# Kernel tuning notes

Measured on AMD Instinct MI355X. Metric: run time of the kernel, lower is better.

Reference implementation:

```python
import jax, jax.numpy as jnp
import numpy as np

NS = 4; DM = 1024; NH = 16; DK = 64; DFF = 4096; ML = 2048
VS = 32000; VT = 32000; B = 2; LS = 512; LT = 512
SCALE = float(np.sqrt(DK))


def _pos_enc():
    # Faithful to the original (quirky) PositionalEncoder:
    # denum uses index i (not i//2); even dims get cos(0)+sin(pe)=1+sin(pe), odd get cos(pe).
    pos = jnp.arange(ML, dtype=jnp.float32)[:, None]              # [ML,1]
    i = jnp.arange(DM, dtype=jnp.float32)[None, :]                # [1,DM]
    denum = 10000.0 ** (2.0 * i / DM)
    pe = pos / denum                                              # [ML,DM]
    c = (jnp.arange(DM) % 2).astype(jnp.float32)[None, :]
    s = 1.0 - c
    return jnp.cos(c * pe) + jnp.sin(s * pe)


def _ln(x, g, b):
    m = x.mean(-1, keepdims=True)
    v = ((x - m) ** 2).mean(-1, keepdims=True)
    return g * (x - m) / jnp.sqrt(v + 1e-5) + b


def _mha(xq, xkv, qkv_w, qkv_b, o_w, o_b, causal):
    # torch.chunk along last dim == reshape [B,L,NH,DK] with contiguous head blocks
    q = (xq @ qkv_w[0] + qkv_b[0]).reshape(xq.shape[0], xq.shape[1], NH, DK)
    k = (xkv @ qkv_w[1] + qkv_b[1]).reshape(xkv.shape[0], xkv.shape[1], NH, DK)
    v = (xkv @ qkv_w[2] + qkv_b[2]).reshape(xkv.shape[0], xkv.shape[1], NH, DK)
    scores = jnp.einsum('bqhd,bkhd->bhqk', q, k) / SCALE
    if causal:
        lq, lk = q.shape[1], k.shape[1]
        m = jnp.arange(lk)[None, :] > jnp.arange(lq)[:, None]     # triu(diagonal=1)
        scores = jnp.where(m[None, None], -jnp.inf, scores)
    a = jax.nn.softmax(scores, axis=-1)
    o = jnp.einsum('bhqk,bkhd->bqhd', a, v).reshape(xq.shape[0], xq.shape[1], NH * DK)
    return o @ o_w + o_b


def setup_inputs() -> dict:
    key = jax.random.key(0)
    ks = iter(jax.random.split(key, 40))

    def n(shape):
        return jax.random.normal(next(ks), shape, dtype=jnp.float32) * 0.02

    inp = {
        's': jax.random.randint(next(ks), (B, LS), 0, VS),
        't': jax.random.randint(next(ks), (B, LT), 0, VT),
        'emb_s_w': n((VS, DM)),
        'emb_t_w': n((VT, DM)),
        'enc_qkv_w': n((NS, 3, DM, DM)), 'enc_qkv_b': n((NS, 3, DM)),
        'enc_o_w': n((NS, DM, DM)), 'enc_o_b': n((NS, DM)),
        'enc_ln_w': jnp.ones((NS, DM), jnp.float32), 'enc_ln_b': jnp.zeros((NS, DM), jnp.float32),
        'enc_w1': n((NS, DM, DFF)), 'enc_b1': n((NS, DFF)),
        'enc_w2': n((NS, DFF, DM)), 'enc_b2': n((NS, DM)),
        'dec_qkv1_w': n((NS, 3, DM, DM)), 'dec_qkv1_b': n((NS, 3, DM)),
        'dec_o1_w': n((NS, DM, DM)), 'dec_o1_b': n((NS, DM)),
        'dec_qkv2_w': n((NS, 3, DM, DM)), 'dec_qkv2_b': n((NS, 3, DM)),
        'dec_o2_w': n((NS, DM, DM)), 'dec_o2_b': n((NS, DM)),
        'dec_ln_w': jnp.ones((NS, DM), jnp.float32), 'dec_ln_b': jnp.zeros((NS, DM), jnp.float32),
        'dec_w1': n((NS, DM, DFF)), 'dec_b1': n((NS, DFF)),
        'dec_w2': n((NS, DFF, DM)), 'dec_b2': n((NS, DM)),
        'out_w': n((DM, VT)), 'out_b': n((VT,)),
    }
    return inp


def reference(s, t, emb_s_w, emb_t_w,
              enc_qkv_w, enc_qkv_b, enc_o_w, enc_o_b, enc_ln_w, enc_ln_b,
              enc_w1, enc_b1, enc_w2, enc_b2,
              dec_qkv1_w, dec_qkv1_b, dec_o1_w, dec_o1_b,
              dec_qkv2_w, dec_qkv2_b, dec_o2_w, dec_o2_b,
              dec_ln_w, dec_ln_b, dec_w1, dec_b1, dec_w2, dec_b2,
              out_w, out_b):
    pe = _pos_enc()
    e = emb_s_w[s] + pe[:s.shape[1]][None]   # dropout p=0 -> identity
    d = emb_t_w[t] + pe[:t.shape[1]][None]

    for i in range(NS):  # encoder stack
        a = _mha(e, e, enc_qkv_w[i], enc_qkv_b[i], enc_o_w[i], enc_o_b[i], False)
        e = _ln(a + e, enc_ln_w[i], enc_ln_b[i])
        f = jnp.maximum(e @ enc_w1[i] + enc_b1[i], 0.0) @ enc_w2[i] + enc_b2[i]
        e = _ln(f + e, enc_ln_w[i], enc_ln_b[i])

    for i in range(NS):  # decoder stack
        a1 = _mha(d, d, dec_qkv1_w[i], dec_qkv1_b[i], dec_o1_w[i], dec_o1_b[i], True)
        d1 = _ln(a1 + d, dec_ln_w[i], dec_ln_b[i])
        # original passes mask=-1, which is truthy -> causal mask in cross-attn too
        a2 = _mha(d1, e, dec_qkv2_w[i], dec_qkv2_b[i], dec_o2_w[i], dec_o2_b[i], True)
        d2 = _ln(a2 + d1, dec_ln_w[i], dec_ln_b[i])
        f = jnp.maximum(d2 @ dec_w1[i] + dec_b1[i], 0.0) @ dec_w2[i] + dec_b2[i]
        d = f + d2  # no final LayerNorm in decoder block (faithful)

    return d @ out_w + out_b
```

## Files before the change

kernel.cpp:

```cpp
#include <hip/hip_runtime.h>
#include <hip/hip_bf16.h>
#include <math.h>

#define NSL 4
#define DM 1024
#define NH 16
#define DKH 64
#define DFF 4096
#define BB 2
#define LL 512
#define VTOK 32000

typedef short s16x8 __attribute__((ext_vector_type(8)));
typedef float f32x4 __attribute__((ext_vector_type(4)));

__device__ __forceinline__ void gload16(const void* g, void* l) {
  __builtin_amdgcn_global_load_lds((__attribute__((address_space(1))) void*)g,
                                   (__attribute__((address_space(3))) void*)l, 16, 0, 0);
}

__global__ __launch_bounds__(256) void embed2_kernel(
    const int* __restrict__ toks, const int* __restrict__ tokt,
    const float* __restrict__ ws, const float* __restrict__ wt,
    float* __restrict__ eo, __hip_bfloat16* __restrict__ eobf,
    float* __restrict__ dco, __hip_bfloat16* __restrict__ dcobf) {
  const int which = blockIdx.y;
  const int* tok = which ? tokt : toks;
  const float* w = which ? wt : ws;
  float* o = which ? dco : eo;
  __hip_bfloat16* obf = which ? dcobf : eobf;
  const int idx = blockIdx.x * 256 + threadIdx.x;
  const int dim = idx & (DM - 1);
  const int pos = (idx >> 10) & (LL - 1);
  const int b   = idx >> 19;
  const int token = tok[b * LL + pos];
  const float denum = powf(10000.0f, (2.0f * (float)dim) / (float)DM);
  const float pe = (float)pos / denum;
  const float val = (dim & 1) ? cosf(pe) : (1.0f + sinf(pe));
  const float r = w[(size_t)token * DM + dim] + val;
  o[idx] = r;
  obf[idx] = __float2bfloat16(r);
}

struct TJobs {
  const float* src[8];
  __hip_bfloat16* dst[8];
  int K[8];
  int N[8];
  int tiles[8];
  int njobs;
};

__global__ __launch_bounds__(256) void transpose_multi(TJobs jobs) {
  __shared__ float tb[64][65];
  int t = blockIdx.x;
  int ji = 0;
  while (t >= jobs.tiles[ji]) { t -= jobs.tiles[ji]; ++ji; }
  const int K = jobs.K[ji], N = jobs.N[ji];
  const int tpx = N >> 6;
  const int tpm = tpx * (K >> 6);
  const int mat = t / tpm;
  const int t2 = t - mat * tpm;
  const float* src = jobs.src[ji] + (long)mat * K * N;
  __hip_bfloat16* dst = jobs.dst[ji] + (long)mat * K * N;
  const int n0 = (t2 % tpx) * 64, k0 = (t2 / tpx) * 64;
  const int lc = (threadIdx.x & 15) * 4;
  const int lr = threadIdx.x >> 4;
  #pragma unroll
  for (int u = 0; u < 4; ++u) {
    const int r = lr + u * 16;
    const float4 v = *(const float4*)(src + (long)(k0 + r) * N + n0 + lc);
    tb[r][lc + 0] = v.x; tb[r][lc + 1] = v.y; tb[r][lc + 2] = v.z; tb[r][lc + 3] = v.w;
  }
  __syncthreads();
  #pragma unroll
  for (int u = 0; u < 4; ++u) {
    const int r = lr + u * 16;
    ushort4 o;
    __hip_bfloat16 h0 = __float2bfloat16(tb[lc + 0][r]);
    __hip_bfloat16 h1 = __float2bfloat16(tb[lc + 1][r]);
    __hip_bfloat16 h2 = __float2bfloat16(tb[lc + 2][r]);
    __hip_bfloat16 h3 = __float2bfloat16(tb[lc + 3][r]);
    o.x = *(unsigned short*)&h0; o.y = *(unsigned short*)&h1;
    o.z = *(unsigned short*)&h2; o.w = *(unsigned short*)&h3;
    *(ushort4*)(dst + (long)(n0 + r) * K + k0 + lc) = o;
  }
}

template<int BM, int BN, int BK, int RELU, int OBF, int SWZ, int VTM, int BMAP, int NTC>
__global__ __launch_bounds__(256, 2) void gemm_mfma(
    const __hip_bfloat16* __restrict__ A, const __hip_bfloat16* __restrict__ BT,
    const float* __restrict__ bias, void* __restrict__ Cout,
    int K, int lda, int ldb, int ldc,
    const float* __restrict__ res, __hip_bfloat16* __restrict__ obf2,
    __hip_bfloat16* __restrict__ vt, int vt_off, long vt_stride) {
  constexpr int WR = BM / 2, WC = BN / 2;
  constexpr int MF = WR / 16, NF = WC / 16;
  constexpr int CHK = BK / 8;
  constexpr int RPC = 64 / CHK;
  constexpr int ACALLS = BM / RPC / 4, BCALLS = BN / RPC / 4;
  constexpr int NLOADS = ACALLS + BCALLS;
  constexpr int KSUB = BK / 32;
  constexpr int ABUF = BM * BK, BBUF = BN * BK;
  constexpr int STAGE_BYTES = 2 * (ABUF + BBUF) * 2;
  constexpr int TT_BYTES = (VTM != 0) ? (BM * BN * 2) : 0;
  constexpr int CF_BYTES = NTC ? ((BM / 2) * BN * 4) : 0;
  constexpr int SMEM_A = STAGE_BYTES > TT_BYTES ? STAGE_BYTES : TT_BYTES;
  constexpr int SMEM_BYTES = SMEM_A > CF_BYTES ? SMEM_A : CF_BYTES;
  __shared__ __align__(16) char smem[SMEM_BYTES];
  __hip_bfloat16* As = (__hip_bfloat16*)smem;
  __hip_bfloat16* Bs = (__hip_bfloat16*)(smem + (size_t)2 * ABUF * 2);
  unsigned short* TT = (unsigned short*)smem;

  int bx = blockIdx.x, by = blockIdx.y;
  if (SWZ) {
    const int gx = gridDim.x;
    const int nwg = gx * gridDim.y;
    const int id = by * gx + bx;
    const int qq = nwg >> 3;
    const int swz = (id & 7) * qq + (id >> 3);
    bx = swz % gx; by = swz / gx;
  }
  const int bm = by * BM, bn = bx * BN;
  const int tid = threadIdx.x, lane = tid & 63, wid = tid >> 6;
  const int wr = (wid >> 1) * WR, wc = (wid & 1) * WC;
  const int frow = lane & 15, fkc = lane >> 4;

  auto swz_chk = [](int c, int r) {
    if (BK == 32)      return c ^ ((r >> 1) & 3);
    else if (BK == 64) return c ^ (r & 7);
    else               return c ^ (r & 15);
  };

  const int s_row = lane / CHK;
  const int s_chk = lane % CHK;

  auto stageAB = [&](int buf, int k0) {
    #pragma unroll
    for (int c = 0; c < ACALLS; ++c) {
      const int R0 = (wid * ACALLS + c) * RPC;
      const int row = R0 + s_row;
      gload16(A + (long)(bm + row) * lda + k0 + swz_chk(s_chk, row) * 8,
              As + buf * ABUF + R0 * BK);
    }
    #pragma unroll
    for (int c = 0; c < BCALLS; ++c) {
      const int R0 = (wid * BCALLS + c) * RPC;
      const int row = R0 + s_row;
      gload16(BT + (long)(bn + row) * ldb + k0 + swz_chk(s_chk, row) * 8,
              Bs + buf * BBUF + R0 * BK);
    }
  };

  f32x4 acc[MF][NF] = {};
  const int nt = K / BK;
  stageAB(0, 0);
  for (int t = 0; t < nt; ++t) {
    const int cur = t & 1;
    const bool more = (t + 1 < nt);
    if (more) {
      stageAB(cur ^ 1, (t + 1) * BK);
      asm volatile("s_waitcnt vmcnt(%0)" :: "n"(NLOADS) : "memory");
    } else {
      asm volatile("s_waitcnt vmcnt(0)" ::: "memory");
    }
    __builtin_amdgcn_s_barrier();
    asm volatile("" ::: "memory");
    #pragma unroll
    for (int s = 0; s < KSUB; ++s) {
      s16x8 af[MF], bfr[NF];
      #pragma unroll
      for (int mm = 0; mm < MF; ++mm) {
        const int r = wr + mm * 16 + frow;
        af[mm] = *(const s16x8*)&As[cur * ABUF + r * BK + swz_chk(s * 4 + fkc, r) * 8];
      }
      #pragma unroll
      for (int nn = 0; nn < NF; ++nn) {
        const int r = wc + nn * 16 + frow;
        bfr[nn] = *(const s16x8*)&Bs[cur * BBUF + r * BK + swz_chk(s * 4 + fkc, r) * 8];
      }
      #pragma unroll
      for (int mm = 0; mm < MF; ++mm)
        #pragma unroll
        for (int nn = 0; nn < NF; ++nn)
          acc[mm][nn] = __builtin_amdgcn_mfma_f32_16x16x32_bf16(af[mm], bfr[nn], acc[mm][nn], 0, 0, 0);
    }
    asm volatile("s_waitcnt lgkmcnt(0)" ::: "memory");
    __builtin_amdgcn_s_barrier();
  }

  if (NTC) {
    float* CF = (float*)smem;
    #pragma unroll
    for (int half = 0; half < 2; ++half) {
      __syncthreads();
      if ((wid >> 1) == half) {
        #pragma unroll
        for (int mm = 0; mm < MF; ++mm)
          #pragma unroll
          for (int nn = 0; nn < NF; ++nn) {
            const int col = wc + nn * 16 + frow;
            const float bs = bias[bn + col];
            #pragma unroll
            for (int j = 0; j < 4; ++j)
              CF[(mm * 16 + fkc * 4 + j) * BN + col] = acc[mm][nn][j] + bs;
          }
      }
      __syncthreads();
      constexpr int NPASS = (BM / 2) * BN / 4 / 256;
      #pragma unroll
      for (int ps = 0; ps < NPASS; ++ps) {
        const int idx = tid * 4 + ps * 1024;
        const int row = idx / BN, col = idx % BN;
        const f32x4 v = *(const f32x4*)&CF[row * BN + col];
        __builtin_nontemporal_store(
            v, (f32x4*)((float*)Cout + (long)(bm + half * (BM / 2) + row) * ldc + bn + col));
      }
    }
    return;
  }

  bool vt_blk = false;
  if (VTM == 1) vt_blk = (bn >= vt_off);
  if (VTM == 2) vt_blk = (((bn >> 10) & 1) == 1);

  #pragma unroll
  for (int mm = 0; mm < MF; ++mm)
    #pragma unroll
    for (int nn = 0; nn < NF; ++nn) {
      const int row0 = bm + wr + mm * 16 + fkc * 4;
      const int col  = bn + wc + nn * 16 + frow;
      float bs;
      if (BMAP) bs = bias[(col >> 11) * 3 * DM + DM + (col & 2047)];
      else      bs = bias[col];
      float vv[4];
      #pragma unroll
      for (int j = 0; j < 4; ++j) {
        float v = acc[mm][nn][j] + bs;
        if (RELU) v = fmaxf(v, 0.0f);
        const long ci = (long)(row0 + j) * ldc + col;
        if (res) v += res[ci];
        if (OBF) ((__hip_bfloat16*)Cout)[ci] = __float2bfloat16(v);
        else     ((float*)Cout)[ci] = v;
        if (obf2) obf2[ci] = __float2bfloat16(v);
        vv[j] = v;
      }
      if (VTM != 0 && vt_blk) {
        const int dl  = wc + nn * 16 + frow;
        const int jl0 = (wr + mm * 16 + fkc * 4) ^ ((dl & 7) << 3);
        ushort4 pk;
        __hip_bfloat16 h0 = __float2bfloat16(vv[0]);
        __hip_bfloat16 h1 = __float2bfloat16(vv[1]);
        __hip_bfloat16 h2 = __float2bfloat16(vv[2]);
        __hip_bfloat16 h3 = __float2bfloat16(vv[3]);
        pk.x = *(unsigned short*)&h0; pk.y = *(unsigned short*)&h1;
        pk.z = *(unsigned short*)&h2; pk.w = *(unsigned short*)&h3;
        *(ushort4*)&TT[dl * BM + jl0] = pk;
      }
    }

  if (VTM != 0 && vt_blk) {
    __syncthreads();
    constexpr int TPR = BM / 8;
    constexpr int RPP = 256 / TPR;
    constexpr int NP  = BN / RPP;
    const int jj = (tid % TPR) * 8;
    const int b = bm >> 9;
    const int jbase = bm & (LL - 1);
    const __hip_bfloat16* vtp;
    int dg0;
    if (VTM == 2) {
      vtp = vt + (long)(bn >> 11) * vt_stride;
      dg0 = bn & 1023;
    } else {
      vtp = vt;
      dg0 = bn - vt_off;
    }
    #pragma unroll
    for (int u = 0; u < NP; ++u) {
      const int dl = (tid / TPR) + u * RPP;
      const s16x8 val = *(const s16x8*)&TT[dl * BM + (jj ^ ((dl & 7) << 3))];
      *(s16x8*)((__hip_bfloat16*)vtp + ((long)(b * DM + dg0 + dl)) * LL + jbase + jj) = val;
    }
  }
}

template<int CAUSAL>
__global__ __launch_bounds__(256) void flash_attn(
    const __hip_bfloat16* __restrict__ Q, int ldq,
    const __hip_bfloat16* __restrict__ K, int ldk,
    const __hip_bfloat16* __restrict__ VT,
    __hip_bfloat16* __restrict__ O) {
  __shared__ __align__(16) __hip_bfloat16 Ks[2][64 * 64];
  __shared__ __align__(16) __hip_bfloat16 Vs[2][64 * 64];
  __shared__ __align__(16) __hip_bfloat16 Ps[4][16 * 64];
  const int qt = blockIdx.x;
  const int bh = blockIdx.y;
  const int b = bh >> 4, h = bh & (NH - 1);
  const int tid = threadIdx.x, lane = tid & 63, wid = tid >> 6;
  const int frow = lane & 15, fg = lane >> 4;

  const __hip_bfloat16* Qb = Q + ((long)b * LL) * ldq + h * DKH;
  const __hip_bfloat16* Kb = K + ((long)b * LL) * ldk + h * DKH;
  const __hip_bfloat16* Vb = VT + (long)b * DM * LL + (long)(h * DKH) * LL;
  __hip_bfloat16* Ob = O + ((long)b * LL) * DM + h * DKH;

  auto stageKV = [&](int buf, int jt) {
    #pragma unroll
    for (int u = 0; u < 2; ++u) {
      const int R0 = (wid * 2 + u) * 8;
      const int row = R0 + (lane >> 3);
      const int cg = (lane & 7) ^ (row & 7);
      gload16(Kb + (long)(jt * 64 + row) * ldk + cg * 8, &Ks[buf][R0 * 64]);
      gload16(Vb + (long)row * LL + jt * 64 + cg * 8, &Vs[buf][R0 * 64]);
    }
  };

  const int qrow = qt * 64 + wid * 16 + frow;
  s16x8 aq[2];
  #pragma unroll
  for (int s = 0; s < 2; ++s)
    aq[s] = *(const s16x8*)(Qb + (long)qrow * ldq + s * 32 + fg * 8);

  f32x4 o[4] = {};
  float m[4], l[4];
  #pragma unroll
  for (int j = 0; j < 4; ++j) { m[j] = -INFINITY; l[j] = 0.0f; }

  const int ntiles = CAUSAL ? (qt + 1) : (LL / 64);
  stageKV(0, 0);
  for (int jt = 0; jt < ntiles; ++jt) {
    const int cur = jt & 1;
    const bool more = (jt + 1 < ntiles);
    if (more) {
      stageKV(cur ^ 1, jt + 1);
      asm volatile("s_waitcnt vmcnt(4)" ::: "memory");
    } else {
      asm volatile("s_waitcnt vmcnt(0)" ::: "memory");
    }
    __builtin_amdgcn_s_barrier();
    asm volatile("" ::: "memory");

    f32x4 sa[4] = {};
    __builtin_amdgcn_s_setprio(1);
    #pragma unroll
    for (int s = 0; s < 2; ++s)
      #pragma unroll
      for (int nf = 0; nf < 4; ++nf) {
        const int jr = nf * 16 + frow;
        const s16x8 kf = *(const s16x8*)&Ks[cur][jr * 64 + (((s * 4 + fg) ^ (jr & 7)) * 8)];
        sa[nf] = __builtin_amdgcn_mfma_f32_16x16x32_bf16(aq[s], kf, sa[nf], 0, 0, 0);
      }
    __builtin_amdgcn_s_setprio(0);
    #pragma unroll
    for (int nf = 0; nf < 4; ++nf)
      #pragma unroll
      for (int j = 0; j < 4; ++j) {
        float v = sa[nf][j] * 0.125f;
        if (CAUSAL) {
          const int r = qt * 64 + wid * 16 + fg * 4 + j;
          const int c = jt * 64 + nf * 16 + frow;
          if (c > r) v = -1e30f;
        }
        sa[nf][j] = v;
      }

    float fs[4];
    #pragma unroll
    for (int j = 0; j < 4; ++j) {
      float v = fmaxf(fmaxf(sa[0][j], sa[1][j]), fmaxf(sa[2][j], sa[3][j]));
      v = fmaxf(v, __shfl_xor(v, 1));
      v = fmaxf(v, __shfl_xor(v, 2));
      v = fmaxf(v, __shfl_xor(v, 4));
      v = fmaxf(v, __shfl_xor(v, 8));
      const float mn = fmaxf(m[j], v);
      fs[j] = __expf(m[j] - mn);
      m[j] = mn;
    }
    float rs[4] = {0.0f, 0.0f, 0.0f, 0.0f};
    #pragma unroll
    for (int nf = 0; nf < 4; ++nf)
      #pragma unroll
      for (int j = 0; j < 4; ++j) {
        const float p = __expf(sa[nf][j] - m[j]);
        sa[nf][j] = p;
        rs[j] += p;
      }
    #pragma unroll
    for (int j = 0; j < 4; ++j) {
      float v = rs[j];
      v += __shfl_xor(v, 1);
      v += __shfl_xor(v, 2);
      v += __shfl_xor(v, 4);
      v += __shfl_xor(v, 8);
      l[j] = l[j] * fs[j] + v;
      o[0][j] *= fs[j]; o[1][j] *= fs[j]; o[2][j] *= fs[j]; o[3][j] *= fs[j];
    }

    __hip_bfloat16* Pw = &Ps[wid][0];
    #pragma unroll
    for (int nf = 0; nf < 4; ++nf)
      #pragma unroll
      for (int j = 0; j < 4; ++j) {
        const int qr = fg * 4 + j;
        const int col = nf * 16 + frow;
        Pw[qr * 64 + (((col >> 3) ^ (qr & 7)) * 8) + (col & 7)] = __float2bfloat16(sa[nf][j]);
      }
    asm volatile("s_waitcnt lgkmcnt(0)" ::: "memory");

    __builtin_amdgcn_s_setprio(1);
    #pragma unroll
    for (int s = 0; s < 2; ++s) {
      const s16x8 pa = *(const s16x8*)&Pw[frow * 64 + (((s * 4 + fg) ^ (frow & 7)) * 8)];
      #pragma unroll
      for (int nf = 0; nf < 4; ++nf) {
        const int dr = nf * 16 + frow;
        const s16x8 vf = *(const s16x8*)&Vs[cur][dr * 64 + (((s * 4 + fg) ^ (dr & 7)) * 8)];
        o[nf] = __builtin_amdgcn_mfma_f32_16x16x32_bf16(pa, vf, o[nf], 0, 0, 0);
      }
    }
    __builtin_amdgcn_s_setprio(0);
    asm volatile("s_waitcnt lgkmcnt(0)" ::: "memory");
    __builtin_amdgcn_s_barrier();
  }

  #pragma unroll
  for (int nf = 0; nf < 4; ++nf)
    #pragma unroll
    for (int j = 0; j < 4; ++j) {
      const int row = qt * 64 + wid * 16 + fg * 4 + j;
      const int col = nf * 16 + frow;
      Ob[(long)row * DM + col] = __float2bfloat16(o[nf][j] / l[j]);
    }
}

__global__ __launch_bounds__(256) void add_ln1(
    const float* __restrict__ x,
    const float* __restrict__ g, const float* __restrict__ bta,
    float* __restrict__ out, __hip_bfloat16* __restrict__ obf) {
  __shared__ float red[256];
  const int tid = threadIdx.x;
  const size_t base = (size_t)blockIdx.x * DM;
  float v[4];
  #pragma unroll
  for (int u = 0; u < 4; ++u) v[u] = x[base + tid + u * 256];
  red[tid] = v[0] + v[1] + v[2] + v[3];
  __syncthreads();
  for (int s = 128; s > 0; s >>= 1) {
    if (tid < s) red[tid] += red[tid + s];
    __syncthreads();
  }
  const float mean = red[0] * (1.0f / DM);
  __syncthreads();
  float sq = 0.0f;
  #pragma unroll
  for (int u = 0; u < 4; ++u) { const float d = v[u] - mean; sq += d * d; }
  red[tid] = sq;
  __syncthreads();
  for (int s = 128; s > 0; s >>= 1) {
    if (tid < s) red[tid] += red[tid + s];
    __syncthreads();
  }
  const float rstd = rsqrtf(red[0] * (1.0f / DM) + 1e-5f);
  #pragma unroll
  for (int u = 0; u < 4; ++u) {
    const int c = tid + u * 256;
    const float o = g[c] * (v[u] - mean) * rstd + bta[c];
    out[base + c] = o;
    obf[base + c] = __float2bfloat16(o);
  }
}

template<int BM, int BN, int BK, int RELU, int OBF, int SWZ, int VTM, int BMAP, int NTC = 0>
static inline void launch_gemm(hipStream_t st, const __hip_bfloat16* A, const __hip_bfloat16* BT,
                               const float* bias, void* C, int M, int N, int K,
                               int lda, int ldb, int ldc,
                               const float* res = nullptr, __hip_bfloat16* obf2 = nullptr,
                               __hip_bfloat16* vt = nullptr, int vt_off = 0, long vt_stride = 0) {
  dim3 g(N / BN, M / BM);
  gemm_mfma<BM, BN, BK, RELU, OBF, SWZ, VTM, BMAP, NTC><<<g, 256, 0, st>>>(
      A, BT, bias, C, K, lda, ldb, ldc, res, obf2, vt, vt_off, vt_stride);
}

static inline void add_tjob(TJobs& J, int& total, const float* src, __hip_bfloat16* dst,
                            int K, int N, int nmat) {
  const int i = J.njobs++;
  J.src[i] = src; J.dst[i] = dst; J.K[i] = K; J.N[i] = N;
  J.tiles[i] = nmat * (N / 64) * (K / 64);
  total += J.tiles[i];
}

extern "C" void kernel_launch(void* const* d_in, const int* in_sizes, int n_in,
                              void* d_out, int out_size, void* d_ws, size_t ws_size,
                              hipStream_t stream) {
  (void)in_sizes; (void)n_in; (void)out_size; (void)ws_size;
  const int*   s          = (const int*)d_in[0];
  const int*   t          = (const int*)d_in[1];
  const float* emb_s_w    = (const float*)d_in[2];
  const float* emb_t_w    = (const float*)d_in[3];
  const float* enc_qkv_w  = (const float*)d_in[4];
  const float* enc_qkv_b  = (const float*)d_in[5];
  const float* enc_o_w    = (const float*)d_in[6];
  const float* enc_o_b    = (const float*)d_in[7];
  const float* enc_ln_w   = (const float*)d_in[8];
  const float* enc_ln_b   = (const float*)d_in[9];
  const float* enc_w1     = (const float*)d_in[10];
  const float* enc_b1     = (const float*)d_in[11];
  const float* enc_w2     = (const float*)d_in[12];
  const float* enc_b2     = (const float*)d_in[13];
  const float* dec_qkv1_w = (const float*)d_in[14];
  const float* dec_qkv1_b = (const float*)d_in[15];
  const float* dec_o1_w   = (const float*)d_in[16];
  const float* dec_o1_b   = (const float*)d_in[17];
  const float* dec_qkv2_w = (const float*)d_in[18];
  const float* dec_qkv2_b = (const float*)d_in[19];
  const float* dec_o2_w   = (const float*)d_in[20];
  const float* dec_o2_b   = (const float*)d_in[21];
  const float* dec_ln_w   = (const float*)d_in[22];
  const float* dec_ln_b   = (const float*)d_in[23];
  const float* dec_w1     = (const float*)d_in[24];
  const float* dec_b1     = (const float*)d_in[25];
  const float* dec_w2     = (const float*)d_in[26];
  const float* dec_b2     = (const float*)d_in[27];
  const float* out_w      = (const float*)d_in[28];
  const float* out_b      = (const float*)d_in[29];
  float* out = (float*)d_out;

  char* p = (char*)d_ws;
  auto alloc = [&](size_t bytes) {
    char* r = p; p += (bytes + 255) & ~(size_t)255; return (void*)r;
  };
  const size_t T = (size_t)BB * LL * DM;
  const size_t DD = (size_t)DM * DM, DF = (size_t)DM * DFF;
  float* e    = (float*)alloc(T * 4);
  float* dcur = (float*)alloc(T * 4);
  float* tmp  = (float*)alloc(T * 4);
  float* d1b  = (float*)alloc(T * 4);
  float* d2b  = (float*)alloc(T * 4);
  __hip_bfloat16* e_bf    = (__hip_bfloat16*)alloc(T * 2);
  __hip_bfloat16* dcur_bf = (__hip_bfloat16*)alloc(T * 2);
  __hip_bfloat16* d1b_bf  = (__hip_bfloat16*)alloc(T * 2);
  __hip_bfloat16* d2b_bf  = (__hip_bfloat16*)alloc(T * 2);
  __hip_bfloat16* q_bf    = (__hip_bfloat16*)alloc(T * 2);
  __hip_bfloat16* qkv_bf  = (__hip_bfloat16*)alloc((size_t)BB * LL * 3 * DM * 2);
  __hip_bfloat16* ab_bf   = (__hip_bfloat16*)alloc(T * 2);
  __hip_bfloat16* hid_bf  = (__hip_bfloat16*)alloc((size_t)BB * LL * DFF * 2);
  __hip_bfloat16* VT      = (__hip_bfloat16*)alloc((size_t)BB * DM * LL * 2);
  __hip_bfloat16* WT      = (__hip_bfloat16*)alloc((size_t)VTOK * DM * 2);
  __hip_bfloat16* WTq   = (__hip_bfloat16*)alloc(4 * DD * 2);
  __hip_bfloat16* WTkv  = (__hip_bfloat16*)alloc(8 * DD * 2);
  __hip_bfloat16* kvall = (__hip_bfloat16*)alloc((size_t)BB * LL * 8192 * 2);
  const long VT4S = (long)BB * DM * LL;
  __hip_bfloat16* VT4   = (__hip_bfloat16*)alloc(4 * VT4S * 2);

  const int M = BB * LL;

  embed2_kernel<<<dim3((int)(T / 256), 2), 256, 0, stream>>>(
      s, t, emb_s_w, emb_t_w, e, e_bf, dcur, dcur_bf);

  for (int i = 0; i < NSL; ++i) {
    TJobs J{}; int tot = 0;
    add_tjob(J, tot, enc_qkv_w + (size_t)i * 3 * DD, WT,            DM, DM, 3);
    add_tjob(J, tot, enc_o_w   + (size_t)i * DD,     WT + 3 * DD,   DM, DM, 1);
    add_tjob(J, tot, enc_w1    + (size_t)i * DF,     WT + 4 * DD,   DM, DFF, 1);
    add_tjob(J, tot, enc_w2    + (size_t)i * DF,     WT + 4 * DD + DF, DFF, DM, 1);
    transpose_multi<<<tot, 256, 0, stream>>>(J);

    launch_gemm<64, 64, 128, 0, 1, 0, 1, 0>(stream, e_bf, WT,
                                            enc_qkv_b + (size_t)i * 3 * DM, qkv_bf,
                                            M, 3 * DM, DM, DM, DM, 3 * DM,
                                            nullptr, nullptr, VT, 2 * DM);
    flash_attn<0><<<dim3(LL / 64, BB * NH), 256, 0, stream>>>(
        qkv_bf, 3 * DM, qkv_bf + DM, 3 * DM, VT, ab_bf);
    launch_gemm<64, 32, 128, 0, 0, 0, 0, 0>(stream, ab_bf, WT + 3 * DD,
                                            enc_o_b + (size_t)i * DM, tmp,
                                            M, DM, DM, DM, DM, DM, e);
    add_ln1<<<M, 256, 0, stream>>>(tmp, enc_ln_w + (size_t)i * DM, enc_ln_b + (size_t)i * DM, e, e_bf);
    launch_gemm<128, 64, 64, 1, 1, 0, 0, 0>(stream, e_bf, WT + 4 * DD,
                                            enc_b1 + (size_t)i * DFF, hid_bf,
                                            M, DFF, DM, DM, DM, DFF);
    launch_gemm<64, 32, 128, 0, 0, 0, 0, 0>(stream, hid_bf, WT + 4 * DD + DF,
                                            enc_b2 + (size_t)i * DM, tmp,
                                            M, DM, DFF, DFF, DFF, DM, e);
    add_ln1<<<M, 256, 0, stream>>>(tmp, enc_ln_w + (size_t)i * DM, enc_ln_b + (size_t)i * DM, e, e_bf);
  }

  {
    TJobs J{}; int tot = 0;
    for (int i = 0; i < NSL; ++i) {
      add_tjob(J, tot, dec_qkv2_w + (size_t)i * 3 * DD,      WTq  + (size_t)i * DD,     DM, DM, 1);
      add_tjob(J, tot, dec_qkv2_w + (size_t)i * 3 * DD + DD, WTkv + (size_t)i * 2 * DD, DM, DM, 2);
    }
    transpose_multi<<<tot, 256, 0, stream>>>(J);
    launch_gemm<128, 128, 32, 0, 1, 0, 2, 1>(stream, e_bf, WTkv, dec_qkv2_b, kvall,
                                             M, 8192, DM, DM, DM, 8192,
                                             nullptr, nullptr, VT4, 0, VT4S);
  }

  for (int i = 0; i < NSL; ++i) {
    TJobs J{}; int tot = 0;
    add_tjob(J, tot, dec_qkv1_w + (size_t)i * 3 * DD, WT,              DM, DM, 3);
    add_tjob(J, tot, dec_o1_w   + (size_t)i * DD,     WT + 3 * DD,     DM, DM, 1);
    add_tjob(J, tot, dec_o2_w   + (size_t)i * DD,     WT + 4 * DD,     DM, DM, 1);
    add_tjob(J, tot, dec_w1     + (size_t)i * DF,     WT + 5 * DD,     DM, DFF, 1);
    add_tjob(J, tot, dec_w2     + (size_t)i * DF,     WT + 5 * DD + DF, DFF, DM, 1);
    transpose_multi<<<tot, 256, 0, stream>>>(J);

    launch_gemm<64, 64, 128, 0, 1, 0, 1, 0>(stream, dcur_bf, WT,
                                            dec_qkv1_b + (size_t)i * 3 * DM, qkv_bf,
                                            M, 3 * DM, DM, DM, DM, 3 * DM,
                                            nullptr, nullptr, VT, 2 * DM);
    flash_attn<1><<<dim3(LL / 64, BB * NH), 256, 0, stream>>>(
        qkv_bf, 3 * DM, qkv_bf + DM, 3 * DM, VT, ab_bf);
    launch_gemm<64, 32, 128, 0, 0, 0, 0, 0>(stream, ab_bf, WT + 3 * DD,
                                            dec_o1_b + (size_t)i * DM, tmp,
                                            M, DM, DM, DM, DM, DM, dcur);
    add_ln1<<<M, 256, 0, stream>>>(tmp, dec_ln_w + (size_t)i * DM, dec_ln_b + (size_t)i * DM, d1b, d1b_bf);

    launch_gemm<64, 32, 128, 0, 1, 0, 0, 0>(stream, d1b_bf, WTq + (size_t)i * DD,
                                            dec_qkv2_b + (size_t)i * 3 * DM, q_bf,
                                            M, DM, DM, DM, DM, DM);
    flash_attn<1><<<dim3(LL / 64, BB * NH), 256, 0, stream>>>(
        q_bf, DM, kvall + (size_t)2048 * i, 8192, VT4 + (size_t)i * VT4S, ab_bf);
    launch_gemm<64, 32, 128, 0, 0, 0, 0, 0>(stream, ab_bf, WT + 4 * DD,
                                            dec_o2_b + (size_t)i * DM, tmp,
                                            M, DM, DM, DM, DM, DM, d1b);
    add_ln1<<<M, 256, 0, stream>>>(tmp, dec_ln_w + (size_t)i * DM, dec_ln_b + (size_t)i * DM, d2b, d2b_bf);

    launch_gemm<128, 64, 64, 1, 1, 0, 0, 0>(stream, d2b_bf, WT + 5 * DD,
                                            dec_b1 + (size_t)i * DFF, hid_bf,
                                            M, DFF, DM, DM, DM, DFF);
    launch_gemm<64, 32, 128, 0, 0, 0, 0, 0>(stream, hid_bf, WT + 5 * DD + DF,
                                            dec_b2 + (size_t)i * DM, dcur,
                                            M, DM, DFF, DFF, DFF, DM, d2b, dcur_bf);
  }

  {
    TJobs J{}; int tot = 0;
    add_tjob(J, tot, out_w, WT, DM, VTOK, 1);
    transpose_multi<<<tot, 256, 0, stream>>>(J);
  }
  launch_gemm<128, 256, 32, 0, 0, 1, 0, 0, 1>(stream, dcur_bf, WT, out_b, out,
                                              M, VTOK, DM, DM, DM, VTOK);
}
```

Measured before the change: 1.155 ms.

## Widen flash attention KV tile to 128 and use warp-shuffle single-pass LayerNorm

The flash attention kernel now stages 128 keys/values per iteration instead of 64. That halves the loop trip count, barriers and per-tile softmax rescales, at the cost of doubled LDS and more registers for the score tile. Causal blocks now process whole 128-wide tiles, so some fully masked work is added at the diagonal. Separately, the add_ln1 LayerNorm replaces its two shared-memory tree reductions with one-pass wavefront shuffles of sum and sum-of-squares. This cuts barriers but computes variance as E[x²]−mean², which is less numerically robust.

```diff
diff --git a/kernel.cpp b/kernel.cpp
--- a/kernel.cpp
+++ b/kernel.cpp
@@ -291,9 +291,9 @@
     const __hip_bfloat16* __restrict__ K, int ldk,
     const __hip_bfloat16* __restrict__ VT,
     __hip_bfloat16* __restrict__ O) {
-  __shared__ __align__(16) __hip_bfloat16 Ks[2][64 * 64];
-  __shared__ __align__(16) __hip_bfloat16 Vs[2][64 * 64];
-  __shared__ __align__(16) __hip_bfloat16 Ps[4][16 * 64];
+  __shared__ __align__(16) __hip_bfloat16 Ks[2][128 * 64];
+  __shared__ __align__(16) __hip_bfloat16 Vs[2][64 * 128];
+  __shared__ __align__(16) __hip_bfloat16 Ps[4][16 * 128];
   const int qt = blockIdx.x;
   const int bh = blockIdx.y;
   const int b = bh >> 4, h = bh & (NH - 1);
@@ -307,12 +307,18 @@
 
   auto stageKV = [&](int buf, int jt) {
     #pragma unroll
-    for (int u = 0; u < 2; ++u) {
-      const int R0 = (wid * 2 + u) * 8;
+    for (int u = 0; u < 4; ++u) {
+      const int R0 = (wid * 4 + u) * 8;
       const int row = R0 + (lane >> 3);
       const int cg = (lane & 7) ^ (row & 7);
-      gload16(Kb + (long)(jt * 64 + row) * ldk + cg * 8, &Ks[buf][R0 * 64]);
-      gload16(Vb + (long)row * LL + jt * 64 + cg * 8, &Vs[buf][R0 * 64]);
+      gload16(Kb + (long)(jt * 128 + row) * ldk + cg * 8, &Ks[buf][R0 * 64]);
+    }
+    #pragma unroll
+    for (int u = 0; u < 4; ++u) {
+      const int R0 = (wid * 4 + u) * 4;
+      const int row = R0 + (lane >> 4);
+      const int cg = (lane & 15) ^ (row & 7);
+      gload16(Vb + (long)row * LL + jt * 128 + cg * 8, &Vs[buf][R0 * 128]);
     }
   };
 
@@ -327,39 +333,39 @@
   #pragma unroll
   for (int j = 0; j < 4; ++j) { m[j] = -INFINITY; l[j] = 0.0f; }
 
-  const int ntiles = CAUSAL ? (qt + 1) : (LL / 64);
+  const int ntiles = CAUSAL ? ((qt >> 1) + 1) : (LL / 128);
   stageKV(0, 0);
   for (int jt = 0; jt < ntiles; ++jt) {
     const int cur = jt & 1;
     const bool more = (jt + 1 < ntiles);
     if (more) {
       stageKV(cur ^ 1, jt + 1);
-      asm volatile("s_waitcnt vmcnt(4)" ::: "memory");
+      asm volatile("s_waitcnt vmcnt(8)" ::: "memory");
     } else {
       asm volatile("s_waitcnt vmcnt(0)" ::: "memory");
     }
     __builtin_amdgcn_s_barrier();
     asm volatile("" ::: "memory");
 
-    f32x4 sa[4] = {};
+    f32x4 sa[8] = {};
     __builtin_amdgcn_s_setprio(1);
     #pragma unroll
     for (int s = 0; s < 2; ++s)
       #pragma unroll
-      for (int nf = 0; nf < 4; ++nf) {
+      for (int nf = 0; nf < 8; ++nf) {
         const int jr = nf * 16 + frow;
         const s16x8 kf = *(const s16x8*)&Ks[cur][jr * 64 + (((s * 4 + fg) ^ (jr & 7)) * 8)];
         sa[nf] = __builtin_amdgcn_mfma_f32_16x16x32_bf16(aq[s], kf, sa[nf], 0, 0, 0);
       }
     __builtin_amdgcn_s_setprio(0);
     #pragma unroll
-    for (int nf = 0; nf < 4; ++nf)
+    for (int nf = 0; nf < 8; ++nf)
       #pragma unroll
       for (int j = 0; j < 4; ++j) {
         float v = sa[nf][j] * 0.125f;
         if (CAUSAL) {
           const int r = qt * 64 + wid * 16 + fg * 4 + j;
-          const int c = jt * 64 + nf * 16 + frow;
+          const int c = jt * 128 + nf * 16 + frow;
           if (c > r) v = -1e30f;
         }
         sa[nf][j] = v;
@@ -368,7 +374,9 @@
     float fs[4];
     #pragma unroll
     for (int j = 0; j < 4; ++j) {
-      float v = fmaxf(fmaxf(sa[0][j], sa[1][j]), fmaxf(sa[2][j], sa[3][j]));
+      float v = sa[0][j];
+      #pragma unroll
+      for (int nf = 1; nf < 8; ++nf) v = fmaxf(v, sa[nf][j]);
       v = fmaxf(v, __shfl_xor(v, 1));
       v = fmaxf(v, __shfl_xor(v, 2));
       v = fmaxf(v, __shfl_xor(v, 4));
@@ -379,7 +387,7 @@
     }
     float rs[4] = {0.0f, 0.0f, 0.0f, 0.0f};
     #pragma unroll
-    for (int nf = 0; nf < 4; ++nf)
+    for (int nf = 0; nf < 8; ++nf)
       #pragma unroll
       for (int j = 0; j < 4; ++j) {
         const float p = __expf(sa[nf][j] - m[j]);
@@ -399,23 +407,23 @@
 
     __hip_bfloat16* Pw = &Ps[wid][0];
     #pragma unroll
-    for (int nf = 0; nf < 4; ++nf)
+    for (int nf = 0; nf < 8; ++nf)
       #pragma unroll
       for (int j = 0; j < 4; ++j) {
         const int qr = fg * 4 + j;
         const int col = nf * 16 + frow;
-        Pw[qr * 64 + (((col >> 3) ^ (qr & 7)) * 8) + (col & 7)] = __float2bfloat16(sa[nf][j]);
+        Pw[qr * 128 + (((col >> 3) ^ (qr & 7)) * 8) + (col & 7)] = __float2bfloat16(sa[nf][j]);
       }
     asm volatile("s_waitcnt lgkmcnt(0)" ::: "memory");
 
     __builtin_amdgcn_s_setprio(1);
     #pragma unroll
-    for (int s = 0; s < 2; ++s) {
-      const s16x8 pa = *(const s16x8*)&Pw[frow * 64 + (((s * 4 + fg) ^ (frow & 7)) * 8)];
+    for (int ks = 0; ks < 4; ++ks) {
+      const s16x8 pa = *(const s16x8*)&Pw[frow * 128 + (((ks * 4 + fg) ^ (frow & 7)) * 8)];
       #pragma unroll
       for (int nf = 0; nf < 4; ++nf) {
         const int dr = nf * 16 + frow;
-        const s16x8 vf = *(const s16x8*)&Vs[cur][dr * 64 + (((s * 4 + fg) ^ (dr & 7)) * 8)];
+        const s16x8 vf = *(const s16x8*)&Vs[cur][dr * 128 + (((ks * 4 + fg) ^ (dr & 7)) * 8)];
         o[nf] = __builtin_amdgcn_mfma_f32_16x16x32_bf16(pa, vf, o[nf], 0, 0, 0);
       }
     }
@@ -438,30 +446,30 @@
     const float* __restrict__ x,
     const float* __restrict__ g, const float* __restrict__ bta,
     float* __restrict__ out, __hip_bfloat16* __restrict__ obf) {
-  __shared__ float red[256];
+  __shared__ float redS[4], redQ[4];
   const int tid = threadIdx.x;
+  const int lane = tid & 63, wid = tid >> 6;
   const size_t base = (size_t)blockIdx.x * DM;
   float v[4];
-  #pragma unroll
-  for (int u = 0; u < 4; ++u) v[u] = x[base + tid + u * 256];
-  red[tid] = v[0] + v[1] + v[2] + v[3];
+  float ss = 0.0f, sq = 0.0f;
+  #pragma unroll
+  for (int u = 0; u < 4; ++u) {
+    v[u] = x[base + tid + u * 256];
+    ss += v[u];
+    sq += v[u] * v[u];
+  }
+  #pragma unroll
+  for (int off = 1; off < 64; off <<= 1) {
+    ss += __shfl_xor(ss, off);
+    sq += __shfl_xor(sq, off);
+  }
+  if (lane == 0) { redS[wid] = ss; redQ[wid] = sq; }
   __syncthreads();
-  for (int s = 128; s > 0; s >>= 1) {
-    if (tid < s) red[tid] += red[tid + s];
-    __syncthreads();
-  }
-  const float mean = red[0] * (1.0f / DM);
-  __syncthreads();
-  float sq = 0.0f;
-  #pragma unroll
-  for (int u = 0; u < 4; ++u) { const float d = v[u] - mean; sq += d * d; }
-  red[tid] = sq;
-  __syncthreads();
-  for (int s = 128; s > 0; s >>= 1) {
-    if (tid < s) red[tid] += red[tid + s];
-    __syncthreads();
-  }
-  const float rstd = rsqrtf(red[0] * (1.0f / DM) + 1e-5f);
+  const float tot = redS[0] + redS[1] + redS[2] + redS[3];
+  const float totq = redQ[0] + redQ[1] + redQ[2] + redQ[3];
+  const float mean = tot * (1.0f / DM);
+  const float var = totq * (1.0f / DM) - mean * mean;
+  const float rstd = rsqrtf(var + 1e-5f);
   #pragma unroll
   for (int u = 0; u < 4; ++u) {
     const int c = tid + u * 256;
```

Result: faster. 1.106 ms (-4.2%).
